# Performance work log

Measured on AMD Instinct MI355X. Metric: run time of the kernel, lower is better.

Reference implementation:

```python
import jax, jax.numpy as jnp
import numpy as np

D = 256; NHEAD = 8; NQ = 300; NLAYERS = 6; NLEV = 3; NPTS = 4
DFF = 1024; NCLS = 80; BS = 16
SPATIAL = ((80, 80), (40, 40), (20, 20))
LM = sum(h * w for h, w in SPATIAL)
DH = D // NHEAD
PARAM_NAMES = ['sa_wq','sa_bq','sa_wk','sa_bk','sa_wv','sa_bv','sa_wo','sa_bo',
               'ln1_g','ln1_b','ln2_g','ln2_b','ln3_g','ln3_b',
               'off_w','off_b','attw_w','attw_b','val_w','val_b','out_w','out_b',
               'ffn_w1','ffn_b1','ffn_w2','ffn_b2',
               'bb_w1','bb_b1','bb_w2','bb_b2','bb_w3','bb_b3',
               'sc_w','sc_b','qp_w1','qp_b1','qp_w2','qp_b2']


def _ln(x, g, b, eps=1e-5):
    m = x.mean(-1, keepdims=True)
    v = ((x - m) ** 2).mean(-1, keepdims=True)
    return (x - m) * jax.lax.rsqrt(v + eps) * g + b


def _mlp2(x, w1, b1, w2, b2):
    # 2-layer MLP, ReLU on hidden only (act_final_layer=False)
    return jnp.maximum(x @ w1 + b1, 0.0) @ w2 + b2


def _inv_sigmoid(x, eps=1e-5):
    x = jnp.clip(x, 0.0, 1.0)
    return jnp.log(jnp.clip(x, eps, None) / jnp.clip(1.0 - x, eps, None))


def _mha(q, k, v, wq, bq, wk, bk, wv, bv, wo, bo):
    B, N, _ = q.shape
    Q = (q @ wq + bq).reshape(B, N, NHEAD, DH)
    K = (k @ wk + bk).reshape(B, N, NHEAD, DH)
    V = (v @ wv + bv).reshape(B, N, NHEAD, DH)
    att = jnp.einsum('bqhd,bkhd->bhqk', Q, K) * (1.0 / np.sqrt(DH))
    att = jax.nn.softmax(att, axis=-1)
    o = jnp.einsum('bhqk,bkhd->bqhd', att, V).reshape(B, N, D)
    return o @ wo + bo


def _bilinear(v, x, y, Hl, Wl):
    # v: [B, Hl*Wl, C]; x, y: [B, M] pixel coords (align_corners=False, zero padding)
    x0 = jnp.floor(x); y0 = jnp.floor(y)
    wx = x - x0; wy = y - y0
    out = 0.0
    for dx, dy, w in ((0, 0, (1 - wx) * (1 - wy)), (1, 0, wx * (1 - wy)),
                      (0, 1, (1 - wx) * wy), (1, 1, wx * wy)):
        xi = x0 + dx; yi = y0 + dy
        valid = (xi >= 0) & (xi < Wl) & (yi >= 0) & (yi < Hl)
        lin = (jnp.clip(yi, 0, Hl - 1) * Wl + jnp.clip(xi, 0, Wl - 1)).astype(jnp.int32)
        g = jnp.take_along_axis(v, lin[..., None], axis=1)
        out = out + g * (w * valid)[..., None]
    return out


def _deform_attn(q, ref, memory, ow, ob, aw, ab, vw, vb, pw, pb):
    # q: [B,NQ,D]; ref: [B,NQ,4] cxcywh in [0,1]; memory: [B,LM,D]
    B = q.shape[0]
    value = (memory @ vw + vb).reshape(B, LM, NHEAD, DH)
    off = (q @ ow + ob).reshape(B, NQ, NHEAD, NLEV, NPTS, 2)
    attw = jax.nn.softmax((q @ aw + ab).reshape(B, NQ, NHEAD, NLEV * NPTS), -1)
    attw = attw.reshape(B, NQ, NHEAD, NLEV, NPTS)
    r = ref[:, :, None, None, None, :]
    loc = r[..., :2] + off / NPTS * r[..., 2:] * 0.5  # [B,NQ,H,LV,P,2]
    start = 0
    acc = 0.0
    for lv, (Hl, Wl) in enumerate(SPATIAL):
        v = value[:, start:start + Hl * Wl]  # [B, Hl*Wl, H, DH]
        v = v.transpose(0, 2, 1, 3).reshape(B * NHEAD, Hl * Wl, DH)
        g = loc[:, :, :, lv]  # [B,NQ,H,P,2]
        x = (g[..., 0] * Wl - 0.5).transpose(0, 2, 1, 3).reshape(B * NHEAD, NQ * NPTS)
        y = (g[..., 1] * Hl - 0.5).transpose(0, 2, 1, 3).reshape(B * NHEAD, NQ * NPTS)
        s = _bilinear(v, x, y, Hl, Wl).reshape(B, NHEAD, NQ, NPTS, DH)
        w = attw[:, :, :, lv].transpose(0, 2, 1, 3)  # [B,H,NQ,P]
        acc = acc + (s * w[..., None]).sum(3)  # [B,H,NQ,DH]
        start += Hl * Wl
    o = acc.transpose(0, 2, 1, 3).reshape(B, NQ, D)
    return o @ pw + pb


def _decoder(tgt, ref_points_unact, memory, p):
    ref_d = jax.nn.sigmoid(ref_points_unact)
    out = tgt
    for i in range(NLAYERS):
        pos = _mlp2(ref_d, p['qp_w1'], p['qp_b1'], p['qp_w2'], p['qp_b2'])
        q = out + pos
        t2 = _mha(q, q, out, p['sa_wq'][i], p['sa_bq'][i], p['sa_wk'][i], p['sa_bk'][i],
                  p['sa_wv'][i], p['sa_bv'][i], p['sa_wo'][i], p['sa_bo'][i])
        out = _ln(out + t2, p['ln1_g'][i], p['ln1_b'][i])
        t2 = _deform_attn(out + pos, ref_d, memory, p['off_w'][i], p['off_b'][i],
                          p['attw_w'][i], p['attw_b'][i], p['val_w'][i], p['val_b'][i],
                          p['out_w'][i], p['out_b'][i])
        out = _ln(out + t2, p['ln2_g'][i], p['ln2_b'][i])
        out = _ln(out + _mlp2(out, p['ffn_w1'][i], p['ffn_b1'][i], p['ffn_w2'][i], p['ffn_b2'][i]),
                  p['ln3_g'][i], p['ln3_b'][i])
        h = jnp.maximum(out @ p['bb_w1'][i] + p['bb_b1'][i], 0.0)
        h = jnp.maximum(h @ p['bb_w2'][i] + p['bb_b2'][i], 0.0)
        delta = h @ p['bb_w3'][i] + p['bb_b3'][i]
        ref_d = jax.nn.sigmoid(delta + _inv_sigmoid(ref_d))
    logits = out @ p['sc_w'][NLAYERS - 1] + p['sc_b'][NLAYERS - 1]
    return ref_d, logits


def setup_inputs():
    key = jax.random.key(0)
    keys = iter(jax.random.split(key, 64))
    def rn(shape, s=0.02):
        return jax.random.normal(next(keys), shape, jnp.float32) * s
    L = NLAYERS
    inp = {
        'tgt': rn((BS, NQ, D), 1.0),
        'ref_points_unact': rn((BS, NQ, 4), 1.0),
        'memory': rn((BS, LM, D), 1.0),
    }
    for n in ['sa_wq', 'sa_wk', 'sa_wv', 'sa_wo', 'val_w', 'out_w', 'bb_w1', 'bb_w2']:
        inp[n] = rn((L, D, D))
    for n in ['sa_bq', 'sa_bk', 'sa_bv', 'sa_bo', 'ln1_b', 'ln2_b', 'ln3_b',
              'val_b', 'out_b', 'ffn_b2', 'bb_b1', 'bb_b2']:
        inp[n] = jnp.zeros((L, D), jnp.float32)
    for n in ['ln1_g', 'ln2_g', 'ln3_g']:
        inp[n] = jnp.ones((L, D), jnp.float32)
    OFF = NHEAD * NLEV * NPTS * 2
    ATT = NHEAD * NLEV * NPTS
    inp['off_w'] = rn((L, D, OFF)); inp['off_b'] = rn((L, OFF), 0.1)
    inp['attw_w'] = rn((L, D, ATT)); inp['attw_b'] = jnp.zeros((L, ATT), jnp.float32)
    inp['ffn_w1'] = rn((L, D, DFF)); inp['ffn_b1'] = jnp.zeros((L, DFF), jnp.float32)
    inp['ffn_w2'] = rn((L, DFF, D))
    inp['bb_w3'] = rn((L, D, 4)); inp['bb_b3'] = jnp.zeros((L, 4), jnp.float32)
    inp['sc_w'] = rn((L, D, NCLS)); inp['sc_b'] = jnp.zeros((L, NCLS), jnp.float32)
    inp['qp_w1'] = rn((4, 2 * D)); inp['qp_b1'] = jnp.zeros((2 * D,), jnp.float32)
    inp['qp_w2'] = rn((2 * D, D)); inp['qp_b2'] = jnp.zeros((D,), jnp.float32)
    return inp


def reference(tgt, ref_points_unact, memory, sa_wq, sa_bq, sa_wk, sa_bk, sa_wv, sa_bv,
              sa_wo, sa_bo, ln1_g, ln1_b, ln2_g, ln2_b, ln3_g, ln3_b, off_w, off_b,
              attw_w, attw_b, val_w, val_b, out_w, out_b, ffn_w1, ffn_b1, ffn_w2, ffn_b2,
              bb_w1, bb_b1, bb_w2, bb_b2, bb_w3, bb_b3, sc_w, sc_b,
              qp_w1, qp_b1, qp_w2, qp_b2):
    _a = dict(locals())
    p = {k: _a[k] for k in PARAM_NAMES}
    ref_d, logits = _decoder(tgt, ref_points_unact, memory, p)
    # eval path: stacked final-layer outputs, shape [1, BS, NQ, 4] and [1, BS, NQ, NCLS]
    return ref_d[None], logits[None]
```

## Files before the change

### kernel.cpp

```cpp
#include <hip/hip_runtime.h>
#include <hip/hip_bf16.h>

typedef __hip_bfloat16 bf16;
typedef short short8 __attribute__((ext_vector_type(8)));
typedef short short4v __attribute__((ext_vector_type(4)));
typedef float float4v __attribute__((ext_vector_type(4)));

#define D_ 256
#define NHEAD_ 8
#define DH_ 32
#define NQ_ 300
#define NLAYERS_ 6
#define DFF_ 1024
#define NCLS_ 80
#define BS_ 16
#define LM_ 8400
#define BN_ (BS_*NQ_)

static __device__ __forceinline__ short f2bf(float x){
    union{float f; unsigned u;} v; v.f = x;
    unsigned r = v.u + 0x7FFF + ((v.u>>16)&1);
    return (short)(r>>16);
}
static __device__ __forceinline__ float bf2f(short s){
    union{unsigned u; float f;} v; v.u = ((unsigned)(unsigned short)s)<<16; return v.f;
}

__global__ __launch_bounds__(256) void bbox_head_kernel(
    const short* __restrict__ curb,
    const short* __restrict__ w1T, const float* __restrict__ b1,
    const short* __restrict__ w2T, const float* __restrict__ b2,
    const float* __restrict__ w3, const float* __restrict__ b3,
    float* __restrict__ refd)
{
    __shared__ short h1[16*264];
    __shared__ float h2[16*260];
    int m0 = blockIdx.x*16;
    int tid = threadIdx.x, lane = tid&63, wave = tid>>6;
    int lr = lane&15, lq = lane>>4;
    int n0 = wave*64;
    short8 af[8];
    #pragma unroll
    for(int kt=0;kt<8;kt++)
        af[kt] = *(const short8*)(curb + (size_t)(m0+lr)*256 + kt*32 + lq*8);
    float4v acc[4];
    #pragma unroll
    for(int nf=0;nf<4;nf++){ acc[nf].x=0.f; acc[nf].y=0.f; acc[nf].z=0.f; acc[nf].w=0.f; }
    #pragma unroll
    for(int kt=0;kt<8;kt++){
        #pragma unroll
        for(int nf=0;nf<4;nf++){
            short8 bfr = *(const short8*)(w1T + (size_t)(n0+nf*16+lr)*256 + kt*32 + lq*8);
            acc[nf] = __builtin_amdgcn_mfma_f32_16x16x32_bf16(af[kt], bfr, acc[nf], 0,0,0);
        }
    }
    #pragma unroll
    for(int nf=0;nf<4;nf++){
        #pragma unroll
        for(int rr=0;rr<4;rr++){
            int row = lq*4+rr, gn = n0+nf*16+lr;
            float v = acc[nf][rr] + b1[gn];
            v = fmaxf(v,0.f);
            ((bf16*)h1)[row*264+gn] = __float2bfloat16(v);
        }
    }
    __syncthreads();
    #pragma unroll
    for(int nf=0;nf<4;nf++){ acc[nf].x=0.f; acc[nf].y=0.f; acc[nf].z=0.f; acc[nf].w=0.f; }
    #pragma unroll
    for(int kt=0;kt<8;kt++){
        short8 a2 = *(const short8*)(&h1[lr*264 + kt*32 + lq*8]);
        #pragma unroll
        for(int nf=0;nf<4;nf++){
            short8 bfr = *(const short8*)(w2T + (size_t)(n0+nf*16+lr)*256 + kt*32 + lq*8);
            acc[nf] = __builtin_amdgcn_mfma_f32_16x16x32_bf16(a2, bfr, acc[nf], 0,0,0);
        }
    }
    #pragma unroll
    for(int nf=0;nf<4;nf++){
        #pragma unroll
        for(int rr=0;rr<4;rr++){
            int row = lq*4+rr, gn = n0+nf*16+lr;
            float v = acc[nf][rr] + b2[gn];
            h2[row*260+gn] = fmaxf(v,0.f);
        }
    }
    __syncthreads();
    {
        int row = tid>>4, sub = tid&15;
        int n = sub>>2, kq = sub&3;
        float p = 0.f;
        const float* hr = h2 + row*260 + kq*64;
        #pragma unroll
        for(int k=0;k<64;k++) p = fmaf(hr[k], w3[(kq*64+k)*4+n], p);
        p += __shfl_xor(p,1);
        p += __shfl_xor(p,2);
        if(kq==0){
            float delta = p + b3[n];
            size_t idx = (size_t)(m0+row)*4+n;
            float x = refd[idx];
            x = fminf(fmaxf(x,0.f),1.f);
            float num = fmaxf(x,1e-5f), den = fmaxf(1.f-x,1e-5f);
            float nd = delta + logf(num/den);
            refd[idx] = 1.f/(1.f+expf(-nd));
        }
    }
}

__global__ __launch_bounds__(256) void pos_mlp_kernel(
    const float* __restrict__ refd, const float* __restrict__ w1, const float* __restrict__ b1,
    const short* __restrict__ w2T, const float* __restrict__ b2,
    const float* __restrict__ cur, float* __restrict__ pos, short* __restrict__ qpb)
{
    __shared__ short hs[32*520];
    __shared__ float rs[32*4];
    int n0 = blockIdx.x*64, m0 = blockIdx.y*32;
    int tid = threadIdx.x;
    if(tid<128) rs[tid] = refd[(size_t)m0*4 + tid];
    __syncthreads();
    {
        int c0 = tid&255;
        float w1r[2][4], b1r[2];
        #pragma unroll
        for(int h=0;h<2;h++){
            int c = c0 + h*256;
            b1r[h] = b1[c];
            #pragma unroll
            for(int k=0;k<4;k++) w1r[h][k] = w1[k*512+c];
        }
        #pragma unroll 4
        for(int j=0;j<64;j++){
            int r = j>>1, h = j&1;
            int c = c0 + h*256;
            float v = 0.f;
            #pragma unroll
            for(int k=0;k<4;k++) v = fmaf(rs[r*4+k], w1r[h][k], v);
            v += b1r[h];
            hs[r*520+c] = f2bf(fmaxf(v,0.f));
        }
    }
    __syncthreads();
    int lane = tid&63, wave = tid>>6;
    int wm = (wave>>1)*16, wn = (wave&1)*32;
    int lr = lane&15, lq = lane>>4;
    float4v acc[2];
    #pragma unroll
    for(int j=0;j<2;j++){ acc[j].x=0.f; acc[j].y=0.f; acc[j].z=0.f; acc[j].w=0.f; }
    short8 pb[2][2];
    #pragma unroll
    for(int ni=0;ni<2;ni++)
        pb[0][ni] = *(const short8*)(w2T + (size_t)(n0+wn+ni*16+lr)*512 + lq*8);
    #pragma unroll
    for(int t=0;t<16;t++){
        const int cur2 = t&1;
        if(t<15){
            #pragma unroll
            for(int ni=0;ni<2;ni++)
                pb[cur2^1][ni] = *(const short8*)(w2T + (size_t)(n0+wn+ni*16+lr)*512 + (t+1)*32 + lq*8);
        }
        short8 a0 = *(const short8*)(&hs[(wm+lr)*520 + t*32 + lq*8]);
        acc[0] = __builtin_amdgcn_mfma_f32_16x16x32_bf16(a0, pb[cur2][0], acc[0], 0,0,0);
        acc[1] = __builtin_amdgcn_mfma_f32_16x16x32_bf16(a0, pb[cur2][1], acc[1], 0,0,0);
    }
    #pragma unroll
    for(int rr=0;rr<4;rr++){
        int gm = m0+wm+lq*4+rr;
        #pragma unroll
        for(int ni=0;ni<2;ni++){
            int gn = n0+wn+ni*16+lr;
            size_t idx = (size_t)gm*256+gn;
            float p = acc[ni][rr] + b2[gn];
            pos[idx] = p;
            qpb[idx] = f2bf(cur[idx] + p);
        }
    }
}

#define LSTR 40

template<int TM, int TN, bool ABF16, bool RELU, bool OUTBF16>
__global__ __launch_bounds__(256) void mfma_gemm_kernel(
    const void* __restrict__ Av, const void* __restrict__ A2v,
    const void* __restrict__ A3v, int nA2lim,
    const short* __restrict__ WT, size_t zWT,
    const float* __restrict__ b0, const float* __restrict__ b1,
    const float* __restrict__ b2, int ns1, int ns2, size_t zB,
    void* __restrict__ Cv, size_t zC, int M, int K, int N, int nxt)
{
    __shared__ short As[2][TM*LSTR];
    __shared__ short Bs[2][TN*LSTR];
    int zz, n0;
    if(nxt){ zz = blockIdx.x / nxt; n0 = (blockIdx.x % nxt)*TN; }
    else   { zz = blockIdx.z;       n0 = blockIdx.x*TN; }
    WT += (size_t)zz*zWT; b0 += (size_t)zz*zB; b1 += (size_t)zz*zB; b2 += (size_t)zz*zB;
    int tid = threadIdx.x;
    int lane = tid&63, wave = tid>>6;
    int m0 = blockIdx.y*TM;
    const int MI = TM/32;
    const int NI = TN/32;
    int wm = (wave>>1)*(TM/2), wn = (wave&1)*(TN/2);
    int lr = lane&15, lq = lane>>4;
    float4v acc[MI][NI];
    #pragma unroll
    for(int i=0;i<MI;i++)
        #pragma unroll
        for(int j=0;j<NI;j++){ acc[i][j].x=0.f; acc[i][j].y=0.f; acc[i][j].z=0.f; acc[i][j].w=0.f; }

    const float* Af; const float* Ad; const short* Ah;
    if(ABF16){
        Ah = (n0 < nA2lim)? (const short*)Av : (const short*)A3v;
        Af=nullptr; Ad=nullptr;
    } else {
        Af = (n0 < nA2lim)? (const float*)Av : (const float*)A3v;
        Ad = (n0 < nA2lim)? (const float*)A2v : nullptr;
        Ah = nullptr;
    }

    short8  rA16[ABF16? TM/64 : 1];
    float4v rAf [ABF16? 1 : TM/32];
    float4v rAd [ABF16? 1 : TM/32];
    short8  rB[TN/64];

    auto LOAD = [&](int k0){
        if constexpr(ABF16){
            #pragma unroll
            for(int it=0; it<TM/64; ++it){
                int idx=(it*256+tid)*8; int r=idx>>5, kk=idx&31; int gm=m0+r;
                short8 v = {};
                if(gm<M) v = *(const short8*)(Ah + (size_t)gm*K + (k0+kk));
                rA16[it]=v;
            }
        } else {
            #pragma unroll
            for(int it=0; it<TM/32; ++it){
                int idx=(it*256+tid)*4; int r=idx>>5, kk=idx&31; int gm=m0+r;
                float4v v; v.x=0.f;v.y=0.f;v.z=0.f;v.w=0.f;
                float4v w; w.x=0.f;w.y=0.f;w.z=0.f;w.w=0.f;
                if(gm<M){
                    v = *(const float4v*)(Af + (size_t)gm*K + (k0+kk));
                    if(Ad) w = *(const float4v*)(Ad + (size_t)gm*K + (k0+kk));
                }
                rAf[it]=v; rAd[it]=w;
            }
        }
        #pragma unroll
        for(int it=0; it<TN/64; ++it){
            int idx=(it*256+tid)*8; int r=idx>>5, kk=idx&31; int gn=n0+r;
            short8 v = {};
            if(gn<N) v = *(const short8*)(WT + (size_t)gn*K + (k0+kk));
            rB[it]=v;
        }
    };
    auto STORE = [&](int buf){
        if constexpr(ABF16){
            #pragma unroll
            for(int it=0; it<TM/64; ++it){
                int idx=(it*256+tid)*8; int r=idx>>5, kk=idx&31;
                *(short8*)(&As[buf][r*LSTR+kk]) = rA16[it];
            }
        } else {
            #pragma unroll
            for(int it=0; it<TM/32; ++it){
                int idx=(it*256+tid)*4; int r=idx>>5, kk=idx&31;
                float4v v = rAf[it];
                if(Ad){ v.x+=rAd[it].x; v.y+=rAd[it].y; v.z+=rAd[it].z; v.w+=rAd[it].w; }
                short4v h; h.x=f2bf(v.x); h.y=f2bf(v.y); h.z=f2bf(v.z); h.w=f2bf(v.w);
                *(short4v*)(&As[buf][r*LSTR+kk]) = h;
            }
        }
        #pragma unroll
        for(int it=0; it<TN/64; ++it){
            int idx=(it*256+tid)*8; int r=idx>>5, kk=idx&31;
            *(short8*)(&Bs[buf][r*LSTR+kk]) = rB[it];
        }
    };

    const int nt = K>>5;
    LOAD(0);
    STORE(0);
    __syncthreads();
    for(int t=0; t<nt; ++t){
        int cb = t&1;
        if(t+1<nt) LOAD((t+1)<<5);
        short8 af[MI], bfr[NI];
        #pragma unroll
        for(int mi=0;mi<MI;mi++) af[mi]  = *(const short8*)(&As[cb][(wm+mi*16+lr)*LSTR + lq*8]);
        #pragma unroll
        for(int ni=0;ni<NI;ni++) bfr[ni] = *(const short8*)(&Bs[cb][(wn+ni*16+lr)*LSTR + lq*8]);
        #pragma unroll
        for(int mi=0;mi<MI;mi++)
            #pragma unroll
            for(int ni=0;ni<NI;ni++)
                acc[mi][ni] = __builtin_amdgcn_mfma_f32_16x16x32_bf16(af[mi], bfr[ni], acc[mi][ni], 0,0,0);
        if(t+1<nt){
            STORE(cb^1);
            __syncthreads();
        }
    }
    float* Cf=(float*)Cv + (size_t)zz*zC; bf16* Ch=(bf16*)Cv + (size_t)zz*zC;
    #pragma unroll
    for(int mi=0;mi<MI;mi++){
        #pragma unroll
        for(int r=0;r<4;r++){
            int gm = m0+wm+mi*16+lq*4+r;
            if(gm>=M) continue;
            #pragma unroll
            for(int ni=0;ni<NI;ni++){
                int gn = n0+wn+ni*16+lr;
                if(gn>=N) continue;
                float bv = (gn<ns1)? b0[gn] : ((gn<ns2)? b1[gn-ns1] : b2[gn-ns2]);
                float v = acc[mi][ni][r] + bv;
                if(RELU) v = fmaxf(v,0.f);
                if(OUTBF16) Ch[(size_t)gm*N+gn]=__float2bfloat16(v);
                else        Cf[(size_t)gm*N+gn]=v;
            }
        }
    }
}

__global__ __launch_bounds__(256) void fused_mha_kernel(
    const short* __restrict__ QKV, short* __restrict__ O)
{
    const int ld = 768;
    int bh = blockIdx.y; int b = bh>>3, h = bh&7;
    int q0 = blockIdx.x*64;
    __shared__ short lds[31104];
    short* Vts = lds;
    short* Qs  = lds + 10368;
    short* Ks  = lds + 12672;
    short* Ps  = lds + 10368;
    int tid = threadIdx.x;
    for(int idx=tid; idx<64*4; idx+=256){
        int r=idx>>2, c8=(idx&3)*8; int gq=q0+r;
        short8 v = {};
        if(gq<NQ_) v = *(const short8*)(QKV + (size_t)(b*NQ_+gq)*ld + h*DH_ + c8);
        *(short8*)(Qs + r*36 + c8) = v;
    }
    for(int idx=tid; idx<304*4; idx+=256){
        int r=idx>>2, c8=(idx&3)*8;
        short8 v = {};
        if(r<NQ_) v = *(const short8*)(QKV + 256 + (size_t)(b*NQ_+r)*ld + h*DH_ + c8);
        *(short8*)(Ks + r*36 + c8) = v;
    }
    for(int idx=tid; idx<320*4; idx+=256){
        int r=idx>>2, c8=(idx&3)*8;
        short8 v = {};
        if(r<NQ_) v = *(const short8*)(QKV + 512 + (size_t)(b*NQ_+r)*ld + h*DH_ + c8);
        #pragma unroll
        for(int j=0;j<8;j++) Vts[(c8+j)*324+r] = v[j];
    }
    __syncthreads();

    int lane = tid&63, wave = tid>>6;
    int lr = lane&15, lq = lane>>4;
    int mrow = wave*16;
    const float scale = 0.17677669529663687f;

    float4v acc[19];
    #pragma unroll
    for(int t=0;t<19;t++){ acc[t].x=0.f; acc[t].y=0.f; acc[t].z=0.f; acc[t].w=0.f; }
    short8 afrag = *(const short8*)(&Qs[(mrow+lr)*36 + lq*8]);
    #pragma unroll
    for(int t=0;t<19;t++){
        short8 bfrag = *(const short8*)(&Ks[(t*16+lr)*36 + lq*8]);
        acc[t] = __builtin_amdgcn_mfma_f32_16x16x32_bf16(afrag, bfrag, acc[t], 0,0,0);
    }
    __syncthreads();

    for(int idx=tid; idx<64*16; idx+=256){
        int r=idx>>4, c=idx&15;
        Ps[r*324 + 304 + c]=0;
    }
    #pragma unroll
    for(int t=0;t<19;t++){
        #pragma unroll
        for(int r=0;r<4;r++) acc[t][r] *= scale;
    }
    if(lr>=12){
        #pragma unroll
        for(int r=0;r<4;r++) acc[18][r] = -1e30f;
    }
    float mx[4];
    #pragma unroll
    for(int r=0;r<4;r++){
        float m = acc[0][r];
        #pragma unroll
        for(int t=1;t<19;t++) m = fmaxf(m, acc[t][r]);
        m = fmaxf(m, __shfl_xor(m,1)); m = fmaxf(m, __shfl_xor(m,2));
        m = fmaxf(m, __shfl_xor(m,4)); m = fmaxf(m, __shfl_xor(m,8));
        mx[r]=m;
    }
    float sum[4] = {0.f,0.f,0.f,0.f};
    #pragma unroll
    for(int t=0;t<19;t++){
        #pragma unroll
        for(int r=0;r<4;r++){
            float p = __expf(acc[t][r]-mx[r]);
            acc[t][r]=p; sum[r]+=p;
        }
    }
    #pragma unroll
    for(int r=0;r<4;r++){
        float s = sum[r];
        s += __shfl_xor(s,1); s += __shfl_xor(s,2);
        s += __shfl_xor(s,4); s += __shfl_xor(s,8);
        sum[r] = 1.f/s;
    }
    #pragma unroll
    for(int t=0;t<19;t++){
        #pragma unroll
        for(int r=0;r<4;r++){
            Ps[(mrow + lq*4 + r)*324 + t*16 + lr] = f2bf(acc[t][r]*sum[r]);
        }
    }
    __syncthreads();
    float4v oacc[2];
    oacc[0].x=0.f;oacc[0].y=0.f;oacc[0].z=0.f;oacc[0].w=0.f;
    oacc[1]=oacc[0];
    #pragma unroll
    for(int kc=0;kc<10;kc++){
        short8 pa = *(const short8*)(&Ps[(mrow+lr)*324 + kc*32 + lq*8]);
        #pragma unroll
        for(int n=0;n<2;n++){
            short8 vb = *(const short8*)(&Vts[(n*16+lr)*324 + kc*32 + lq*8]);
            oacc[n] = __builtin_amdgcn_mfma_f32_16x16x32_bf16(pa, vb, oacc[n], 0,0,0);
        }
    }
    #pragma unroll
    for(int n=0;n<2;n++){
        #pragma unroll
        for(int r=0;r<4;r++){
            int gq = q0 + mrow + lq*4 + r;
            if(gq<NQ_)
                O[((size_t)(b*NQ_+gq))*D_ + h*DH_ + n*16 + lr] = f2bf(oacc[n][r]);
        }
    }
}

#define NTD 74
struct TD { const float* src; unsigned dstoff; int K, N, base; };
struct TAll { TD d[NTD]; };

__global__ __launch_bounds__(256) void transpose_all_kernel(TAll p, short* __restrict__ WTb){
    int blk = blockIdx.x;
    int di = 0;
    #pragma unroll 1
    for(int i=0;i<NTD;i++){ if(blk >= p.d[i].base) di = i; }
    TD d = p.d[di];
    int rel = blk - d.base;
    int ntx = (d.N+31)/32;
    int tn = (rel % ntx)*32, tk = (rel / ntx)*32;
    __shared__ float t[32][33];
    int tx = threadIdx.x&31, ty = threadIdx.x>>5;
    for(int i=0;i<32;i+=8){
        int k = tk+ty+i, n = tn+tx;
        t[ty+i][tx] = (k<d.K && n<d.N)? d.src[(size_t)k*d.N+n] : 0.f;
    }
    __syncthreads();
    short* out = WTb + d.dstoff;
    for(int i=0;i<32;i+=8){
        int n = tn+ty+i, k = tk+tx;
        if(n<d.N && k<d.K) out[(size_t)n*d.K+k] = f2bf(t[tx][ty+i]);
    }
}

__global__ void copy_kernel(const float* __restrict__ a, float* __restrict__ o,
                            short* __restrict__ cb, int n){
    int i = blockIdx.x*blockDim.x+threadIdx.x;
    if(i<n){ float v=a[i]; o[i]=v; cb[i]=f2bf(v); }
}
__global__ void cvt_f32_bf16_kernel(const float* __restrict__ a, short* __restrict__ o, int n4){
    int i = blockIdx.x*blockDim.x+threadIdx.x;
    if(i<n4){
        float4v v = *(const float4v*)(a + (size_t)i*4);
        short4v h; h.x=f2bf(v.x); h.y=f2bf(v.y); h.z=f2bf(v.z); h.w=f2bf(v.w);
        *(short4v*)(o + (size_t)i*4) = h;
    }
}
__global__ void sigmoid_init_kernel(const float* __restrict__ a, float* __restrict__ o, int n){
    int i = blockIdx.x*blockDim.x+threadIdx.x;
    if(i<n){ float x=a[i]; o[i]=1.f/(1.f+expf(-x)); }
}
__global__ void write_out_kernel(const float* __restrict__ refd, const float* __restrict__ logits, float* __restrict__ out){
    int i = blockIdx.x*blockDim.x+threadIdx.x;
    if(i<BN_*4) out[i]=refd[i];
    else if(i<BN_*4+BN_*NCLS_) out[i]=logits[i-BN_*4];
}

__global__ __launch_bounds__(256) void ln_residual_kernel(
    float* __restrict__ cur, const short* __restrict__ t2b,
    const float* __restrict__ g, const float* __restrict__ b,
    short* __restrict__ cb, const float* __restrict__ pa)
{
    int row = blockIdx.x; int c = threadIdx.x;
    size_t idx = (size_t)row*D_+c;
    float x = cur[idx] + bf2f(t2b[idx]);
    float v1 = x, v2 = x*x;
    #pragma unroll
    for(int o=32;o>0;o>>=1){ v1 += __shfl_down(v1,o,64); v2 += __shfl_down(v2,o,64); }
    __shared__ float s1[4], s2[4], st[2];
    int wid=c>>6, lane=c&63;
    if(lane==0){ s1[wid]=v1; s2[wid]=v2; }
    __syncthreads();
    if(c==0){
        float a=0,d=0;
        #pragma unroll
        for(int i=0;i<4;i++){a+=s1[i]; d+=s2[i];}
        st[0]=a/(float)D_; st[1]=d/(float)D_;
    }
    __syncthreads();
    float m=st[0], var=st[1]-m*m;
    float y = (x-m)*rsqrtf(var+1e-5f)*g[c] + b[c];
    cur[idx]=y;
    if(cb) cb[idx] = f2bf(pa? y + pa[idx] : y);
}

__global__ __launch_bounds__(256) void deform_sample_kernel(
    const float* __restrict__ refd, const float* __restrict__ oab,
    const bf16* __restrict__ value, short* __restrict__ outacc)
{
    int row = blockIdx.x; int b = row/NQ_;
    int tid = threadIdx.x; int h = tid>>5, c = tid&31;
    __shared__ float so[192], sa[96], sr[4];
    if(tid<192) so[tid]=oab[(size_t)row*288+tid];
    if(tid<96)  sa[tid]=oab[(size_t)row*288+192+tid];
    if(tid<4)   sr[tid]=refd[(size_t)row*4+tid];
    __syncthreads();
    if(tid<8){
        float* p = sa + tid*12;
        float m=-1e30f;
        #pragma unroll
        for(int i2=0;i2<12;i2++) m=fmaxf(m,p[i2]);
        float s=0.f;
        #pragma unroll
        for(int i2=0;i2<12;i2++){ float e=__expf(p[i2]-m); p[i2]=e; s+=e; }
        float inv=1.f/s;
        #pragma unroll
        for(int i2=0;i2<12;i2++) p[i2]*=inv;
    }
    __syncthreads();
    float cx=sr[0], cy=sr[1], rw=sr[2], rh=sr[3];
    const int HS[3]={80,40,20}, WS[3]={80,40,20}, ST[3]={0,6400,8000};
    float acc=0.f;
    const bf16* vb = value + (size_t)b*LM_*D_ + h*DH_ + c;
    for(int lv=0;lv<3;lv++){
        int Hl=HS[lv], Wl=WS[lv], st=ST[lv];
        #pragma unroll
        for(int pt=0;pt<4;pt++){
            int oi = ((h*3+lv)*4+pt)*2;
            float ox=so[oi], oy=so[oi+1];
            float wa=sa[h*12+lv*4+pt];
            float lx = cx + ox*0.25f*rw*0.5f;
            float ly = cy + oy*0.25f*rh*0.5f;
            float x = lx*(float)Wl - 0.5f, y = ly*(float)Hl - 0.5f;
            float x0f=floorf(x), y0f=floorf(y);
            float wx=x-x0f, wy=y-y0f;
            int x0=(int)x0f, y0=(int)y0f;
            #pragma unroll
            for(int dy=0;dy<2;dy++){
                #pragma unroll
                for(int dx=0;dx<2;dx++){
                    int xi=x0+dx, yi=y0+dy;
                    if(xi>=0 && xi<Wl && yi>=0 && yi<Hl){
                        float w = (dx? wx : 1.f-wx)*(dy? wy : 1.f-wy);
                        int lin = yi*Wl+xi;
                        acc += __bfloat162float(vb[(size_t)(st+lin)*D_]) * (w*wa);
                    }
                }
            }
        }
    }
    outacc[(size_t)row*D_+tid]=f2bf(acc);
}

static void g64x(const void*A, const void*A2, const void*A3, int nA2lim,
                 const short*WT, const float*b0, const float*b1, const float*b2,
                 int ns1, int ns2, void*C, int M,int K,int N,
                 bool abf16, bool relu, bool outbf, hipStream_t s){
    dim3 g((N+63)/64,(M+63)/64,1);
    #define CALLG(AB,RL,OB) mfma_gemm_kernel<64,64,AB,RL,OB><<<g,256,0,s>>>(A,A2,A3,nA2lim,WT,0,b0,b1,b2,ns1,ns2,0,C,0,M,K,N,0)
    if(abf16){
        if(relu){ if(outbf) CALLG(true,true,true);  else CALLG(true,true,false); }
        else    { if(outbf) CALLG(true,false,true); else CALLG(true,false,false); }
    } else {
        if(relu){ if(outbf) CALLG(false,true,true);  else CALLG(false,true,false); }
        else    { if(outbf) CALLG(false,false,true); else CALLG(false,false,false); }
    }
    #undef CALLG
}
static void g64b(const short*A, const short*WT, const float*b, void*C,
                 int M,int K,int N, hipStream_t s){
    g64x(A,nullptr,A,1<<30,WT,b,b,b,N,N+1,C,M,K,N,true,false,true,s);
}
static int ntiles(int K,int N){ return ((N+31)/32)*((K+31)/32); }

extern "C" void kernel_launch(void* const* d_in, const int* in_sizes, int n_in,
                              void* d_out, int out_size, void* d_ws, size_t ws_size,
                              hipStream_t stream) {
    const float* tgt   = (const float*)d_in[0];
    const float* rpu   = (const float*)d_in[1];
    const float* mem   = (const float*)d_in[2];
    const float* sa_wq = (const float*)d_in[3];
    const float* sa_wk = (const float*)d_in[4];
    const float* sa_wv = (const float*)d_in[5];
    const float* sa_wo = (const float*)d_in[6];
    const float* val_w = (const float*)d_in[7];
    const float* out_w = (const float*)d_in[8];
    const float* bb_w1 = (const float*)d_in[9];
    const float* bb_w2 = (const float*)d_in[10];
    const float* sa_bq = (const float*)d_in[11];
    const float* sa_bk = (const float*)d_in[12];
    const float* sa_bv = (const float*)d_in[13];
    const float* sa_bo = (const float*)d_in[14];
    const float* ln1_b = (const float*)d_in[15];
    const float* ln2_b = (const float*)d_in[16];
    const float* ln3_b = (const float*)d_in[17];
    const float* val_b = (const float*)d_in[18];
    const float* out_b = (const float*)d_in[19];
    const float* ffn_b2= (const float*)d_in[20];
    const float* bb_b1 = (const float*)d_in[21];
    const float* bb_b2 = (const float*)d_in[22];
    const float* ln1_g = (const float*)d_in[23];
    const float* ln2_g = (const float*)d_in[24];
    const float* ln3_g = (const float*)d_in[25];
    const float* off_w = (const float*)d_in[26];
    const float* off_b = (const float*)d_in[27];
    const float* attw_w= (const float*)d_in[28];
    const float* attw_b= (const float*)d_in[29];
    const float* ffn_w1= (const float*)d_in[30];
    const float* ffn_b1= (const float*)d_in[31];
    const float* ffn_w2= (const float*)d_in[32];
    const float* bb_w3 = (const float*)d_in[33];
    const float* bb_b3 = (const float*)d_in[34];
    const float* sc_w  = (const float*)d_in[35];
    const float* sc_b  = (const float*)d_in[36];
    const float* qp_w1 = (const float*)d_in[37];
    const float* qp_b1 = (const float*)d_in[38];
    const float* qp_w2 = (const float*)d_in[39];
    const float* qp_b2 = (const float*)d_in[40];

    const size_t BND = (size_t)BN_*D_;
    const size_t USZ = (size_t)BN_*DFF_;
    const size_t LMD = (size_t)BS_*LM_*D_;
    const size_t LSZ = 1122304;

    float* ws   = (float*)d_ws;
    float* cur  = ws;
    float* pos  = cur + BND;
    float* refd = pos + BND;
    float* U    = refd + (size_t)BN_*4;
    short* tmp16 = (short*)(U + USZ);
    short* t216  = tmp16 + BND;
    short* WT    = t216 + BND;
    short* qp2T  = WT + 6*LSZ;
    short* scT   = qp2T + 131072;
    short* qpb   = scT + 20480;
    short* X     = qpb + BND;
    short* QKVh16 = (short*)U;
    float* offsb  = U;
    short* ffnh16 = (short*)U;
    float* logitsb= U;
    short* curb = tmp16;

    size_t offX = (size_t)((char*)X - (char*)d_ws);
    int vmode;
    if(ws_size >= offX + 7*LMD*2)      vmode = 3;
    else if(ws_size >= offX + 6*LMD*2) vmode = 2;
    else if(ws_size >= offX + 4*LMD)   vmode = 1;
    else                               vmode = 0;
    short* memT   = X;
    short* values = (vmode==3)? X + LMD : X;
    short* value1 = X + LMD;
    short* value0 = X;

    const int nBN_D = (int)BND;
    copy_kernel<<<(nBN_D+255)/256,256,0,stream>>>(tgt, cur, curb, nBN_D);
    sigmoid_init_kernel<<<(BN_*4+255)/256,256,0,stream>>>(rpu, refd, BN_*4);
    if(vmode==1 || vmode==3){
        int n4 = (int)(LMD/4);
        cvt_f32_bf16_kernel<<<(n4+255)/256,256,0,stream>>>(mem, memT, n4);
    }

    {
        TAll tp; int base=0; int di=0;
        const size_t offs[12] = { 0,65536,131072,196608,262144,327680,
                                  393216,442368,466944,729088,991232,1056768 };
        const int Ks[12] = { 256,256,256,256,256,256,256,256,256,1024,256,256 };
        const int Ns[12] = { 256,256,256,256,256,256,192,96,1024,256,256,256 };
        for(int l=0;l<NLAYERS_;l++){
            const float* srcs[12] = { sa_wq+(size_t)l*D_*D_, sa_wk+(size_t)l*D_*D_, sa_wv+(size_t)l*D_*D_,
                                      sa_wo+(size_t)l*D_*D_, val_w+(size_t)l*D_*D_, out_w+(size_t)l*D_*D_,
                                      off_w+(size_t)l*D_*192, attw_w+(size_t)l*D_*96,
                                      ffn_w1+(size_t)l*D_*DFF_, ffn_w2+(size_t)l*DFF_*D_,
                                      bb_w1+(size_t)l*D_*D_, bb_w2+(size_t)l*D_*D_ };
            for(int j=0;j<12;j++){
                tp.d[di] = { srcs[j], (unsigned)(l*LSZ + offs[j]), Ks[j], Ns[j], base };
                base += ntiles(Ks[j],Ns[j]); di++;
            }
        }
        tp.d[di] = { qp_w2, (unsigned)(6*LSZ), 512, 256, base }; base += ntiles(512,256); di++;
        tp.d[di] = { sc_w + (size_t)(NLAYERS_-1)*D_*NCLS_, (unsigned)(6*LSZ+131072), 256, 80, base }; base += ntiles(256,80); di++;
        transpose_all_kernel<<<base,256,0,stream>>>(tp, WT);
    }

    if(vmode==3){
        dim3 g(12,1050,1);
        mfma_gemm_kernel<128,128,true,false,true><<<g,256,0,stream>>>(
            memT,nullptr,memT,1<<30, WT+262144, LSZ,
            val_b,val_b,val_b, 256,257, 256, values, LMD, BS_*LM_, D_, D_, 2);
    } else if(vmode==2){
        dim3 g(12,1050,1);
        mfma_gemm_kernel<128,128,false,false,true><<<g,256,0,stream>>>(
            mem,nullptr,mem,1<<30, WT+262144, LSZ,
            val_b,val_b,val_b, 256,257, 256, values, LMD, BS_*LM_, D_, D_, 2);
    }

    for(int i=0;i<NLAYERS_;i++){
        const bf16* value_i;
        if(vmode>=2) value_i = (const bf16*)(values + (size_t)i*LMD);
        else {
            dim3 g(2,1050,1);
            if(vmode==1){
                mfma_gemm_kernel<128,128,true,false,true><<<g,256,0,stream>>>(
                    memT,nullptr,memT,1<<30, WT+i*LSZ+262144, 0,
                    val_b+(size_t)i*D_,val_b,val_b, 256,257, 0, value1, 0, BS_*LM_, D_, D_, 0);
                value_i = (const bf16*)value1;
            } else {
                mfma_gemm_kernel<128,128,false,false,true><<<g,256,0,stream>>>(
                    mem,nullptr,mem,1<<30, WT+i*LSZ+262144, 0,
                    val_b+(size_t)i*D_,val_b,val_b, 256,257, 0, value0, 0, BS_*LM_, D_, D_, 0);
                value_i = (const bf16*)value0;
            }
        }
        pos_mlp_kernel<<<dim3(4,150),256,0,stream>>>(refd, qp_w1, qp_b1, qp2T, qp_b2,
                                                     cur, pos, qpb);
        g64x(qpb, nullptr, curb, 512, WT+i*LSZ,
             sa_bq+(size_t)i*D_, sa_bk+(size_t)i*D_, sa_bv+(size_t)i*D_, 256, 512,
             QKVh16, BN_, D_, 768, true,false,true, stream);
        {
            dim3 g((NQ_+63)/64, BS_*NHEAD_);
            fused_mha_kernel<<<g,256,0,stream>>>(QKVh16, tmp16);
        }
        g64b(tmp16, WT+i*LSZ+196608, sa_bo+(size_t)i*D_, t216, BN_, D_, D_, stream);
        ln_residual_kernel<<<BN_,256,0,stream>>>(cur, t216, ln1_g+(size_t)i*D_, ln1_b+(size_t)i*D_, qpb, pos);
        g64x(qpb, nullptr, qpb, 1<<30, WT+i*LSZ+393216,
             off_b+(size_t)i*192, attw_b+(size_t)i*96, attw_b+(size_t)i*96, 192, 288,
             offsb, BN_, D_, 288, true,false,false, stream);
        deform_sample_kernel<<<BN_,256,0,stream>>>(refd, offsb, value_i, tmp16);
        g64b(tmp16, WT+i*LSZ+327680, out_b+(size_t)i*D_, t216, BN_, D_, D_, stream);
        ln_residual_kernel<<<BN_,256,0,stream>>>(cur, t216, ln2_g+(size_t)i*D_, ln2_b+(size_t)i*D_, curb, nullptr);
        g64x(curb,nullptr,curb,1<<30, WT+i*LSZ+466944, ffn_b1+(size_t)i*DFF_,ffn_b1,ffn_b1, DFF_,DFF_+1,
             ffnh16, BN_, D_, DFF_, true,true,true, stream);
        g64x(ffnh16,nullptr,ffnh16,1<<30, WT+i*LSZ+729088, ffn_b2+(size_t)i*D_,ffn_b2,ffn_b2, 256,257,
             t216, BN_, DFF_, D_, true,false,true, stream);
        ln_residual_kernel<<<BN_,256,0,stream>>>(cur, t216, ln3_g+(size_t)i*D_, ln3_b+(size_t)i*D_, curb, nullptr);
        bbox_head_kernel<<<BN_/16,256,0,stream>>>(curb,
            WT+i*LSZ+991232, bb_b1+(size_t)i*D_,
            WT+i*LSZ+1056768, bb_b2+(size_t)i*D_,
            bb_w3+(size_t)i*D_*4, bb_b3+(size_t)i*4, refd);
    }
    g64x(curb,nullptr,curb,1<<30, scT, sc_b+(size_t)(NLAYERS_-1)*NCLS_,sc_b,sc_b, NCLS_,NCLS_+1,
         logitsb, BN_, D_, NCLS_, true,false,false, stream);
    int tot = BN_*4 + BN_*NCLS_;
    write_out_kernel<<<(tot+255)/256,256,0,stream>>>(refd, logitsb, (float*)d_out);
}
```

Baseline: 2.072 ms.

## Fuse output-projection GEMMs with residual add and LayerNorm

Adds a gemm_ln_kernel that computes a 16-row by 256-column GEMM tile per 512-thread block with MFMA, adds bias and the residual, and performs LayerNorm in shared memory. It replaces the three GEMM plus ln_residual_kernel pairs per layer (self-attention out-proj, deformable out-proj, FFN second layer). This removes the bf16 intermediate round trip through global memory and three kernel launches per layer. In exchange, each block covers only 16 rows and reloads the full weight matrix from global/L2 with no LDS staging, so the GEMM part may be less efficient than the 64x64 tiled kernel.

```diff
diff --git a/kernel.cpp b/kernel.cpp
--- a/kernel.cpp
+++ b/kernel.cpp
@@ -24,6 +24,93 @@
 }
 static __device__ __forceinline__ float bf2f(short s){
     union{unsigned u; float f;} v; v.u = ((unsigned)(unsigned short)s)<<16; return v.f;
+}
+
+template<int KD>
+__global__ __launch_bounds__(512) void gemm_ln_kernel(
+    const short* __restrict__ A, const short* __restrict__ WT,
+    const float* __restrict__ bias, const float* __restrict__ g, const float* __restrict__ b,
+    float* __restrict__ cur, short* __restrict__ cb, const float* __restrict__ pa)
+{
+    __shared__ float xs_[16*260];
+    int m0 = blockIdx.x*16;
+    int tid = threadIdx.x, lane = tid&63, wave = tid>>6;
+    int lr = lane&15, lq = lane>>4;
+    int n0 = wave*32;
+    float4v acc[2];
+    #pragma unroll
+    for(int j=0;j<2;j++){ acc[j].x=0.f; acc[j].y=0.f; acc[j].z=0.f; acc[j].w=0.f; }
+    short8 pb[2][2];
+    #pragma unroll
+    for(int ni=0;ni<2;ni++)
+        pb[0][ni] = *(const short8*)(WT + (size_t)(n0+ni*16+lr)*KD + lq*8);
+    if constexpr(KD==256){
+        short8 af[8];
+        #pragma unroll
+        for(int kt=0;kt<8;kt++)
+            af[kt] = *(const short8*)(A + (size_t)(m0+lr)*KD + kt*32 + lq*8);
+        #pragma unroll
+        for(int kt=0;kt<8;kt++){
+            const int c2 = kt&1;
+            if(kt<7){
+                #pragma unroll
+                for(int ni=0;ni<2;ni++)
+                    pb[c2^1][ni] = *(const short8*)(WT + (size_t)(n0+ni*16+lr)*KD + (kt+1)*32 + lq*8);
+            }
+            acc[0] = __builtin_amdgcn_mfma_f32_16x16x32_bf16(af[kt], pb[c2][0], acc[0], 0,0,0);
+            acc[1] = __builtin_amdgcn_mfma_f32_16x16x32_bf16(af[kt], pb[c2][1], acc[1], 0,0,0);
+        }
+    } else {
+        short8 a0 = *(const short8*)(A + (size_t)(m0+lr)*KD + lq*8);
+        #pragma unroll
+        for(int kt=0;kt<KD/32;kt++){
+            const int c2 = kt&1;
+            short8 a1 = a0;
+            if(kt<KD/32-1){
+                a1 = *(const short8*)(A + (size_t)(m0+lr)*KD + (kt+1)*32 + lq*8);
+                #pragma unroll
+                for(int ni=0;ni<2;ni++)
+                    pb[c2^1][ni] = *(const short8*)(WT + (size_t)(n0+ni*16+lr)*KD + (kt+1)*32 + lq*8);
+            }
+            acc[0] = __builtin_amdgcn_mfma_f32_16x16x32_bf16(a0, pb[c2][0], acc[0], 0,0,0);
+            acc[1] = __builtin_amdgcn_mfma_f32_16x16x32_bf16(a0, pb[c2][1], acc[1], 0,0,0);
+            a0 = a1;
+        }
+    }
+    #pragma unroll
+    for(int ni=0;ni<2;ni++){
+        #pragma unroll
+        for(int rr=0;rr<4;rr++){
+            int row = lq*4+rr, col = n0+ni*16+lr;
+            float v = bf2f(f2bf(acc[ni][rr] + bias[col]));
+            xs_[row*260+col] = cur[(size_t)(m0+row)*256+col] + v;
+        }
+    }
+    __syncthreads();
+    #pragma unroll
+    for(int r=0;r<2;r++){
+        int row = wave*2+r; int grow = m0+row;
+        float a=0.f, d=0.f; float xv[4];
+        #pragma unroll
+        for(int p=0;p<4;p++){
+            float v1 = xs_[row*260 + p*64 + lane];
+            xv[p]=v1;
+            float v2 = v1*v1;
+            #pragma unroll
+            for(int o=32;o>0;o>>=1){ v1 += __shfl_down(v1,o,64); v2 += __shfl_down(v2,o,64); }
+            a += __shfl(v1,0,64); d += __shfl(v2,0,64);
+        }
+        float m = a/(float)D_, var = d/(float)D_ - m*m;
+        float rs = rsqrtf(var+1e-5f);
+        #pragma unroll
+        for(int p=0;p<4;p++){
+            int c = p*64+lane;
+            size_t idx = (size_t)grow*256+c;
+            float y = (xv[p]-m)*rs*g[c]+b[c];
+            cur[idx]=y;
+            if(cb) cb[idx] = f2bf(pa? y+pa[idx] : y);
+        }
+    }
 }
 
 __global__ __launch_bounds__(256) void bbox_head_kernel(
@@ -487,34 +574,6 @@
     else if(i<BN_*4+BN_*NCLS_) out[i]=logits[i-BN_*4];
 }
 
-__global__ __launch_bounds__(256) void ln_residual_kernel(
-    float* __restrict__ cur, const short* __restrict__ t2b,
-    const float* __restrict__ g, const float* __restrict__ b,
-    short* __restrict__ cb, const float* __restrict__ pa)
-{
-    int row = blockIdx.x; int c = threadIdx.x;
-    size_t idx = (size_t)row*D_+c;
-    float x = cur[idx] + bf2f(t2b[idx]);
-    float v1 = x, v2 = x*x;
-    #pragma unroll
-    for(int o=32;o>0;o>>=1){ v1 += __shfl_down(v1,o,64); v2 += __shfl_down(v2,o,64); }
-    __shared__ float s1[4], s2[4], st[2];
-    int wid=c>>6, lane=c&63;
-    if(lane==0){ s1[wid]=v1; s2[wid]=v2; }
-    __syncthreads();
-    if(c==0){
-        float a=0,d=0;
-        #pragma unroll
-        for(int i=0;i<4;i++){a+=s1[i]; d+=s2[i];}
-        st[0]=a/(float)D_; st[1]=d/(float)D_;
-    }
-    __syncthreads();
-    float m=st[0], var=st[1]-m*m;
-    float y = (x-m)*rsqrtf(var+1e-5f)*g[c] + b[c];
-    cur[idx]=y;
-    if(cb) cb[idx] = f2bf(pa? y + pa[idx] : y);
-}
-
 __global__ __launch_bounds__(256) void deform_sample_kernel(
     const float* __restrict__ refd, const float* __restrict__ oab,
     const bf16* __restrict__ value, short* __restrict__ outacc)
@@ -587,10 +646,6 @@
         else    { if(outbf) CALLG(false,false,true); else CALLG(false,false,false); }
     }
     #undef CALLG
-}
-static void g64b(const short*A, const short*WT, const float*b, void*C,
-                 int M,int K,int N, hipStream_t s){
-    g64x(A,nullptr,A,1<<30,WT,b,b,b,N,N+1,C,M,K,N,true,false,true,s);
 }
 static int ntiles(int K,int N){ return ((N+31)/32)*((K+31)/32); }
 
@@ -741,19 +796,18 @@
             dim3 g((NQ_+63)/64, BS_*NHEAD_);
             fused_mha_kernel<<<g,256,0,stream>>>(QKVh16, tmp16);
         }
-        g64b(tmp16, WT+i*LSZ+196608, sa_bo+(size_t)i*D_, t216, BN_, D_, D_, stream);
-        ln_residual_kernel<<<BN_,256,0,stream>>>(cur, t216, ln1_g+(size_t)i*D_, ln1_b+(size_t)i*D_, qpb, pos);
+        gemm_ln_kernel<256><<<BN_/16,512,0,stream>>>(tmp16, WT+i*LSZ+196608,
+            sa_bo+(size_t)i*D_, ln1_g+(size_t)i*D_, ln1_b+(size_t)i*D_, cur, qpb, pos);
         g64x(qpb, nullptr, qpb, 1<<30, WT+i*LSZ+393216,
              off_b+(size_t)i*192, attw_b+(size_t)i*96, attw_b+(size_t)i*96, 192, 288,
              offsb, BN_, D_, 288, true,false,false, stream);
         deform_sample_kernel<<<BN_,256,0,stream>>>(refd, offsb, value_i, tmp16);
-        g64b(tmp16, WT+i*LSZ+327680, out_b+(size_t)i*D_, t216, BN_, D_, D_, stream);
-        ln_residual_kernel<<<BN_,256,0,stream>>>(cur, t216, ln2_g+(size_t)i*D_, ln2_b+(size_t)i*D_, curb, nullptr);
+        gemm_ln_kernel<256><<<BN_/16,512,0,stream>>>(tmp16, WT+i*LSZ+327680,
+            out_b+(size_t)i*D_, ln2_g+(size_t)i*D_, ln2_b+(size_t)i*D_, cur, curb, nullptr);
         g64x(curb,nullptr,curb,1<<30, WT+i*LSZ+466944, ffn_b1+(size_t)i*DFF_,ffn_b1,ffn_b1, DFF_,DFF_+1,
              ffnh16, BN_, D_, DFF_, true,true,true, stream);
-        g64x(ffnh16,nullptr,ffnh16,1<<30, WT+i*LSZ+729088, ffn_b2+(size_t)i*D_,ffn_b2,ffn_b2, 256,257,
-             t216, BN_, DFF_, D_, true,false,true, stream);
-        ln_residual_kernel<<<BN_,256,0,stream>>>(cur, t216, ln3_g+(size_t)i*D_, ln3_b+(size_t)i*D_, curb, nullptr);
+        gemm_ln_kernel<1024><<<BN_/16,512,0,stream>>>(ffnh16, WT+i*LSZ+729088,
+            ffn_b2+(size_t)i*D_, ln3_g+(size_t)i*D_, ln3_b+(size_t)i*D_, cur, curb, nullptr);
         bbox_head_kernel<<<BN_/16,256,0,stream>>>(curb,
             WT+i*LSZ+991232, bb_b1+(size_t)i*D_,
             WT+i*LSZ+1056768, bb_b2+(size_t)i*D_,
```

Result: slower. 2.242 ms (+8.2%).
